# Optimization experiments

Measured on AMD Instinct MI355X. Metric: run time of the kernel, lower is better.

## Reference

```python
import jax, jax.numpy as jnp
import numpy as np
import math

EPS = 1e-20
TEMP = 0.07


def _affinity(x1, x2, n):
    # x1, x2: (B, C, T-1, N+1); use only the first n (non-dustbin) nodes
    A = jnp.einsum('bctn,bctm->btnm', x1[..., :n], x2[..., :n])  # (B,T-1,n,n)
    # entropy of row-normalized affinities (intended math of Categorical(probs=A[b,t,k]).entropy())
    p = A / A.sum(-1, keepdims=True)
    ent = -(p * jnp.log(jnp.maximum(p, EPS))).sum(-1)            # (B,T-1,n)
    dustbin_w = 1.0 / math.log(n)
    A = jnp.concatenate([A, (ent * dustbin_w)[..., None]], axis=-1)  # (B,T-1,n,n+1)
    dust_row = -A.sum(-2)[:, :, None, :]                              # (B,T-1,1,n+1)
    A = jnp.concatenate([A, dust_row], axis=2)                        # (B,T-1,n+1,n+1)
    A = A.at[:, :, -1, -1].set(0.0)
    return A


def _l2norm(x, axis):
    return x / jnp.maximum(jnp.linalg.norm(x, axis=axis, keepdims=True), 1e-12)


def _forward(feats_raw, dust_raw, W_self, b_self, W_dust, b_dust):
    B, N, Cenc, T = feats_raw.shape
    # selfsim head: Linear over channel dim, then L2-normalize features
    f = jnp.einsum('bnct,cd->bndt', feats_raw, W_self) + b_self[None, None, :, None]
    f = _l2norm(f, axis=2)                      # (B,N,128,T)
    q = jnp.transpose(f, (0, 2, 3, 1))          # (B,128,T,N)
    d = jnp.einsum('bct,cd->bdt', dust_raw, W_dust) + b_dust[None, :, None]
    d = _l2norm(d, axis=1)                      # (B,128,T)
    q = jnp.concatenate([q, d[..., None]], axis=-1)  # (B,128,T,N+1)

    Af = _affinity(q[:, :, :-1], q[:, :, 1:], N)
    qf = jnp.flip(q, axis=2)
    Ab = _affinity(qf[:, :, :-1], qf[:, :, 1:], N)

    A12 = jax.nn.softmax(Af / TEMP, axis=-1)    # (B,T-1,M,M)
    A21 = jax.nn.softmax(Ab / TEMP, axis=-1)

    M = N + 1
    tgt = jnp.tile(jnp.arange(M), B)            # (B*M,)
    rows = jnp.arange(B * M)
    left = A12[:, 0]
    right = A21[:, T - 2]
    losses = []
    for i in range(1, T - 1):                   # fixed small loop over time steps
        left = left @ A12[:, i]
        right = A21[:, T - 2 - i] @ right
        AA = left @ right                       # (B,M,M) palindrome walk
        logits = jnp.log(AA + EPS).reshape(-1, M)
        ls = jax.nn.log_softmax(logits, axis=-1)
        losses.append(-ls[rows, tgt].mean())
    loss = sum(losses) / len(losses)
    return q, loss


def setup_inputs() -> dict:
    key = jax.random.key(0)
    ks = jax.random.split(key, 4)
    B, N, C, T, D = 4, 784, 512, 8, 128
    return {
        'feats_raw': jax.random.normal(ks[0], (B, N, C, T), dtype=jnp.float32),
        'dust_raw': jax.random.normal(ks[1], (B, C, T), dtype=jnp.float32),
        'W_self': jax.random.normal(ks[2], (C, D), dtype=jnp.float32) * 0.05,
        'b_self': jnp.zeros((D,), dtype=jnp.float32),
        'W_dust': jax.random.normal(ks[3], (C, D), dtype=jnp.float32) * 0.05,
        'b_dust': jnp.zeros((D,), dtype=jnp.float32),
    }


def reference(feats_raw, dust_raw, W_self, b_self, W_dust, b_dust):
    return _forward(feats_raw, dust_raw, W_self, b_self, W_dust, b_dust)
```

## Files before the change

kernel.cpp:

```cpp
#include <hip/hip_runtime.h>
#include <hip/hip_bf16.h>
#include <math.h>

constexpr int Bc = 4;
constexpr int Nc = 784;
constexpr int Cc = 512;
constexpr int Tc = 8;
constexpr int Dc = 128;
constexpr int Mc = 785;
constexpr int TM1 = 7;
constexpr int Pp = 832;
constexpr int Qrows = 896;
constexpr float TEMP = 0.07f;

typedef __attribute__((ext_vector_type(4))) float f32x4;
typedef __attribute__((ext_vector_type(8))) unsigned short u16x8;
typedef __attribute__((ext_vector_type(8))) __bf16 bf16x8;

__device__ __forceinline__ unsigned short f2bf(float v) {
    __hip_bfloat16 h = __float2bfloat16(v);
    return __builtin_bit_cast(unsigned short, h);
}
__device__ __forceinline__ float bf2f(unsigned short u) {
    return __builtin_bit_cast(float, (unsigned int)u << 16);
}

__device__ __forceinline__ void gload16(const void* g, void* l) {
    __builtin_amdgcn_global_load_lds(
        (const __attribute__((address_space(1))) unsigned int*)g,
        (__attribute__((address_space(3))) unsigned int*)l, 16, 0, 0);
}

template<int LD>
__device__ __forceinline__ void mfma_tile_loop(const unsigned short* __restrict__ A,
                                               const unsigned short* __restrict__ BT,
                                               unsigned short* __restrict__ As,
                                               unsigned short* __restrict__ Bs,
                                               int i0, int j0, int tid,
                                               f32x4 (&acc)[4][4])
{
    const int lane = tid & 63, w = tid >> 6;
    const int wr = w >> 1, wc = w & 1;
    const int g = lane >> 4, lr = lane & 15;

    for (int k0 = 0; k0 < LD; k0 += 64) {
        __syncthreads();
        #pragma unroll
        for (int q = 0; q < 4; ++q) {
            int L16 = q * 256 + tid;
            int r = L16 >> 3;
            int csw = ((L16 & 7) << 4) ^ ((r & 7) << 4);
            const char* ga = (const char*)(A  + (size_t)(i0 + r) * LD + k0) + csw;
            const char* gb = (const char*)(BT + (size_t)(j0 + r) * LD + k0) + csw;
            gload16(ga, As + (size_t)L16 * 8);
            gload16(gb, Bs + (size_t)L16 * 8);
        }
        __syncthreads();
        #pragma unroll
        for (int ks = 0; ks < 2; ++ks) {
            bf16x8 af[4], bf[4];
            #pragma unroll
            for (int m = 0; m < 4; ++m) {
                int r = wr * 64 + m * 16 + lr;
                int cb = (ks * 64 + g * 16) ^ ((r & 7) << 4);
                af[m] = __builtin_bit_cast(bf16x8, *(const u16x8*)((const char*)As + r * 128 + cb));
            }
            #pragma unroll
            for (int n = 0; n < 4; ++n) {
                int r = wc * 64 + n * 16 + lr;
                int cb = (ks * 64 + g * 16) ^ ((r & 7) << 4);
                bf[n] = __builtin_bit_cast(bf16x8, *(const u16x8*)((const char*)Bs + r * 128 + cb));
            }
            #pragma unroll
            for (int m = 0; m < 4; ++m)
                #pragma unroll
                for (int n = 0; n < 4; ++n)
                    acc[m][n] = __builtin_amdgcn_mfma_f32_16x16x32_bf16(af[m], bf[n], acc[m][n], 0, 0, 0);
        }
    }
}

__device__ __forceinline__ float blockReduceSum(float v, float* sbuf) {
    #pragma unroll
    for (int off = 32; off; off >>= 1) v += __shfl_down(v, off, 64);
    __syncthreads();
    if ((threadIdx.x & 63) == 0) sbuf[threadIdx.x >> 6] = v;
    __syncthreads();
    return sbuf[0] + sbuf[1] + sbuf[2] + sbuf[3];
}
__device__ __forceinline__ float blockReduceMax(float v, float* sbuf) {
    #pragma unroll
    for (int off = 32; off; off >>= 1) v = fmaxf(v, __shfl_down(v, off, 64));
    __syncthreads();
    if ((threadIdx.x & 63) == 0) sbuf[threadIdx.x >> 6] = v;
    __syncthreads();
    return fmaxf(fmaxf(sbuf[0], sbuf[1]), fmaxf(sbuf[2], sbuf[3]));
}

__global__ __launch_bounds__(256) void k_pack(const float* __restrict__ feats,
                                              unsigned int* __restrict__ Abf32)
{
    __shared__ float lds[Cc * 9];
    int bid = blockIdx.x;
    int b = bid / Nc, n = bid % Nc;
    const float* src = feats + (size_t)(b * Nc + n) * Cc * Tc;
    int tid = threadIdx.x;
    for (int i = tid; i < Cc * Tc; i += 256) lds[(i >> 3) * 9 + (i & 7)] = src[i];
    __syncthreads();
    #pragma unroll
    for (int t = 0; t < Tc; ++t) {
        size_t row = (size_t)(b * Tc + t) * Nc + n;
        float v0 = lds[(2 * tid) * 9 + t];
        float v1 = lds[(2 * tid + 1) * 9 + t];
        unsigned int pk = (unsigned int)f2bf(v0) | ((unsigned int)f2bf(v1) << 16);
        Abf32[row * (Cc / 2) + tid] = pk;
    }
}

__global__ __launch_bounds__(256) void k_packw(const float* __restrict__ Wself,
                                               const float* __restrict__ Wdust,
                                               unsigned short* __restrict__ WTb)
{
    __shared__ float tile[64][65];
    int which = blockIdx.z;
    const float* W = which ? Wdust : Wself;
    unsigned short* O = WTb + (size_t)which * Dc * Cc;
    int d0 = blockIdx.x * 64, c0 = blockIdx.y * 64;
    int tx = threadIdx.x & 63, ty = threadIdx.x >> 6;
    #pragma unroll
    for (int y = 0; y < 64; y += 4) tile[y + ty][tx] = W[(size_t)(c0 + y + ty) * Dc + d0 + tx];
    __syncthreads();
    #pragma unroll
    for (int y = 0; y < 64; y += 4) O[(size_t)(d0 + y + ty) * Cc + c0 + tx] = f2bf(tile[tx][y + ty]);
}

__global__ __launch_bounds__(256, 3) void k_gemm_proj(const unsigned short* __restrict__ A,
                                                      const unsigned short* __restrict__ BT,
                                                      const float* __restrict__ bias,
                                                      float* __restrict__ Cf)
{
    __shared__ __align__(16) unsigned short As[128 * 64];
    __shared__ __align__(16) unsigned short Bs[128 * 64];
    const int i0 = blockIdx.y * 128;
    const int tid = threadIdx.x, lane = tid & 63, w = tid >> 6;
    const int wr = w >> 1, wc = w & 1;
    const int g = lane >> 4, lr = lane & 15;

    f32x4 acc[4][4] = {};
    mfma_tile_loop<Cc>(A, BT, As, Bs, i0, 0, tid, acc);

    #pragma unroll
    for (int n = 0; n < 4; ++n) {
        int col = wc * 64 + n * 16 + lr;
        float bv = bias[col];
        #pragma unroll
        for (int m = 0; m < 4; ++m)
            #pragma unroll
            for (int j = 0; j < 4; ++j) {
                int row = i0 + wr * 64 + m * 16 + g * 4 + j;
                Cf[(size_t)row * Dc + col] = acc[m][n][j] + bv;
            }
    }
}

__global__ __launch_bounds__(128) void k_dustproj(const float* __restrict__ dust,
                                                  const float* __restrict__ Wdust,
                                                  const float* __restrict__ bdust,
                                                  unsigned short* __restrict__ qTb,
                                                  float* __restrict__ qout)
{
    __shared__ float sdust[Cc];
    __shared__ float red[2];
    int bt = blockIdx.x;
    int b = bt >> 3, t = bt & 7;
    int tid = threadIdx.x;
    for (int i = tid; i < Cc; i += 128) sdust[i] = dust[((size_t)b * Cc + i) * Tc + t];
    __syncthreads();
    float acc = 0.f;
    for (int c = 0; c < Cc; ++c) acc += sdust[c] * Wdust[(size_t)c * Dc + tid];
    acc += bdust[tid];
    float s = acc * acc;
    #pragma unroll
    for (int off = 32; off; off >>= 1) s += __shfl_down(s, off, 64);
    if ((tid & 63) == 0) red[tid >> 6] = s;
    __syncthreads();
    float inv = 1.f / fmaxf(sqrtf(red[0] + red[1]), 1e-12f);
    float qv = acc * inv;
    qTb[((size_t)bt * Qrows + Nc) * Dc + tid] = f2bf(qv);
    qout[(((size_t)b * Dc + tid) * Tc + t) * Mc + Nc] = qv;
}

__global__ __launch_bounds__(256) void k_norm(const float* __restrict__ fbuf,
                                              unsigned short* __restrict__ qTb,
                                              float* __restrict__ qout)
{
    __shared__ float lds[64][129];
    __shared__ float nrm[64][4];
    __shared__ float inv[64];
    int bt = blockIdx.y;
    int b = bt >> 3, t = bt & 7;
    int n0 = blockIdx.x * 64;
    int tid = threadIdx.x;
    #pragma unroll
    for (int q = 0; q < 8; ++q) {
        int i = q * 256 + tid;
        int nl = i >> 5, d4 = i & 31;
        f32x4 v = {};
        if (n0 + nl < Nc) v = *(const f32x4*)(fbuf + ((size_t)bt * Nc + n0 + nl) * Dc + d4 * 4);
        *(f32x4*)(&lds[nl][d4 * 4]) = v;
    }
    __syncthreads();
    {
        int r = tid & 63, p = tid >> 6;
        float s = 0.f;
        #pragma unroll
        for (int j = 0; j < 32; ++j) { float v = lds[r][p * 32 + j]; s += v * v; }
        nrm[r][p] = s;
    }
    __syncthreads();
    if (tid < 64) inv[tid] = 1.f / fmaxf(sqrtf(nrm[tid][0] + nrm[tid][1] + nrm[tid][2] + nrm[tid][3]), 1e-12f);
    __syncthreads();
    unsigned int* qT32 = (unsigned int*)(qTb + (size_t)bt * Qrows * Dc);
    #pragma unroll
    for (int q = 0; q < 16; ++q) {
        int i = q * 256 + tid;
        int nl = i >> 6, dp = i & 63;
        if (n0 + nl < Nc) {
            float iv = inv[nl];
            unsigned int pk = (unsigned int)f2bf(lds[nl][2 * dp] * iv)
                            | ((unsigned int)f2bf(lds[nl][2 * dp + 1] * iv) << 16);
            qT32[((size_t)(n0 + nl) * Dc >> 1) + dp] = pk;
        }
    }
    int nl = tid & 63;
    if (n0 + nl < Nc) {
        float iv = inv[nl];
        #pragma unroll
        for (int dd = 0; dd < Dc; dd += 4) {
            int d = dd + (tid >> 6);
            qout[(((size_t)b * Dc + d) * Tc + t) * Mc + n0 + nl] = lds[nl][d] * iv;
        }
    }
}

__global__ __launch_bounds__(256) void k_affinity(const unsigned short* __restrict__ qTb,
                                                  unsigned short* __restrict__ P12h,
                                                  unsigned short* __restrict__ P21h,
                                                  float* __restrict__ cs12,
                                                  float* __restrict__ cs21,
                                                  float wconst)
{
    constexpr float INVT = 1.0f / TEMP;
    const size_t MMp = (size_t)Pp * Pp;
    int f = blockIdx.x;
    int xcd = f & 7, slot = f >> 3;
    int grp = xcd + 8 * (slot / 49);
    int strip = slot % 49;
    int side = grp >= 28 ? 1 : 0;
    int bt = grp - side * 28;
    int b = bt / TM1, t = bt % TM1;
    const unsigned short *Aq, *Bq;
    unsigned short* OUT;
    float* cs;
    if (side == 0) {
        Aq = qTb + (size_t)(b * Tc + t)     * Qrows * Dc;
        Bq = qTb + (size_t)(b * Tc + t + 1) * Qrows * Dc;
        OUT = P12h + (size_t)bt * MMp;
        cs  = cs12 + (size_t)bt * Pp;
    } else {
        Aq = qTb + (size_t)(b * Tc + 7 - t) * Qrows * Dc;
        Bq = qTb + (size_t)(b * Tc + 6 - t) * Qrows * Dc;
        OUT = P21h + (size_t)bt * MMp;
        cs  = cs21 + (size_t)bt * Pp;
    }
    const int r0 = strip * 16;
    const int tid = threadIdx.x, lane = tid & 63, w = tid >> 6;
    const int g = lane >> 4, lr = lane & 15;

    f32x4 acc[13] = {};
    #pragma unroll
    for (int ks = 0; ks < 4; ++ks) {
        bf16x8 af = __builtin_bit_cast(bf16x8,
            *(const u16x8*)(Aq + (size_t)(r0 + lr) * Dc + ks * 32 + g * 8));
        bf16x8 bfr[7];
        #pragma unroll
        for (int tt = 0; tt < 7; ++tt)
            if (w * 13 + tt < 49)
                bfr[tt] = __builtin_bit_cast(bf16x8,
                    *(const u16x8*)(Bq + (size_t)((w * 13 + tt) * 16 + lr) * Dc + ks * 32 + g * 8));
        #pragma unroll
        for (int tt = 0; tt < 7; ++tt)
            if (w * 13 + tt < 49)
                acc[tt] = __builtin_amdgcn_mfma_f32_16x16x32_bf16(af, bfr[tt], acc[tt], 0, 0, 0);
        #pragma unroll
        for (int tt = 7; tt < 13; ++tt)
            if (w * 13 + tt < 49)
                bfr[tt - 7] = __builtin_bit_cast(bf16x8,
                    *(const u16x8*)(Bq + (size_t)((w * 13 + tt) * 16 + lr) * Dc + ks * 32 + g * 8));
        #pragma unroll
        for (int tt = 7; tt < 13; ++tt)
            if (w * 13 + tt < 49)
                acc[tt] = __builtin_amdgcn_mfma_f32_16x16x32_bf16(af, bfr[tt - 7], acc[tt], 0, 0, 0);
    }

    __shared__ float sred[16][4][2];
    __shared__ float rowsum[16], invZ[16], entP[16];

    float rs[4] = {0.f, 0.f, 0.f, 0.f};
    #pragma unroll
    for (int tt = 0; tt < 13; ++tt) {
        int gt = w * 13 + tt;
        if (gt < 49) {
            float c = 0.f;
            #pragma unroll
            for (int j = 0; j < 4; ++j) {
                float a = acc[tt][j];
                rs[j] += a;
                c += a;
            }
            c += __shfl_xor(c, 16, 64);
            c += __shfl_xor(c, 32, 64);
            if (g == 0) atomicAdd(&cs[gt * 16 + lr], c);
        }
    }
    #pragma unroll
    for (int off = 1; off <= 8; off <<= 1) {
        #pragma unroll
        for (int j = 0; j < 4; ++j) rs[j] += __shfl_xor(rs[j], off, 64);
    }
    if (lr == 0) {
        #pragma unroll
        for (int j = 0; j < 4; ++j) sred[g * 4 + j][w][0] = rs[j];
    }
    __syncthreads();
    if (tid < 16)
        rowsum[tid] = sred[tid][0][0] + sred[tid][1][0] + sred[tid][2][0] + sred[tid][3][0];
    __syncthreads();

    float invr[4];
    #pragma unroll
    for (int j = 0; j < 4; ++j) invr[j] = 1.0f / rowsum[g * 4 + j];
    float en[4] = {0.f, 0.f, 0.f, 0.f}, es[4] = {0.f, 0.f, 0.f, 0.f};
    #pragma unroll
    for (int tt = 0; tt < 13; ++tt) {
        if (w * 13 + tt < 49) {
            #pragma unroll
            for (int j = 0; j < 4; ++j) {
                float a = acc[tt][j];
                float e = __expf(a * INVT);
                es[j] += e;
                float p = a * invr[j];
                en[j] -= p * __logf(fmaxf(p, 1e-20f));
                acc[tt][j] = e;
            }
        }
    }
    #pragma unroll
    for (int off = 1; off <= 8; off <<= 1) {
        #pragma unroll
        for (int j = 0; j < 4; ++j) {
            es[j] += __shfl_xor(es[j], off, 64);
            en[j] += __shfl_xor(en[j], off, 64);
        }
    }
    if (lr == 0) {
        #pragma unroll
        for (int j = 0; j < 4; ++j) { sred[g * 4 + j][w][0] = es[j]; sred[g * 4 + j][w][1] = en[j]; }
    }
    __syncthreads();
    if (tid < 16) {
        float esum = sred[tid][0][0] + sred[tid][1][0] + sred[tid][2][0] + sred[tid][3][0];
        float ent  = sred[tid][0][1] + sred[tid][1][1] + sred[tid][2][1] + sred[tid][3][1];
        float ez  = __expf(ent * wconst * INVT);
        float Z   = esum + ez;
        float iz  = 1.0f / Z;
        invZ[tid] = iz;
        entP[tid] = ez * iz;
    }
    __syncthreads();

    float izl[4];
    #pragma unroll
    for (int j = 0; j < 4; ++j) izl[j] = invZ[g * 4 + j];
    #pragma unroll
    for (int tt = 0; tt < 13; ++tt) {
        int gt = w * 13 + tt;
        int col = gt * 16 + lr;
        #pragma unroll
        for (int j = 0; j < 4; ++j) {
            int row = r0 + g * 4 + j;
            if (gt < 49)
                OUT[(size_t)row * Pp + col] = f2bf(acc[tt][j] * izl[j]);
            else if (col != 784)
                OUT[(size_t)row * Pp + col] = 0;
        }
    }
    if (tid < 16) OUT[(size_t)(r0 + tid) * Pp + 784] = f2bf(entP[tid]);
}

__global__ __launch_bounds__(256) void k_dustrow(const float* __restrict__ cs12,
                                                 const float* __restrict__ cs21,
                                                 unsigned short* __restrict__ P12h,
                                                 unsigned short* __restrict__ P21h)
{
    constexpr float INVT = 1.0f / TEMP;
    const size_t MMp = (size_t)Pp * Pp;
    int bt = blockIdx.x, side = blockIdx.y;
    const float* cs = (side ? cs21 : cs12) + (size_t)bt * Pp;
    unsigned short* OUT = (side ? P21h : P12h) + (size_t)bt * MMp;
    __shared__ float sbuf[4];
    int tid = threadIdx.x;
    float v[4];
    #pragma unroll
    for (int k = 0; k < 4; ++k) {
        int j = tid + k * 256;
        float val = -INFINITY;
        if (j < Nc)       val = -cs[j] * INVT;
        else if (j == Nc) val = 0.f;
        v[k] = val;
    }
    float mx = fmaxf(fmaxf(v[0], v[1]), fmaxf(v[2], v[3]));
    mx = blockReduceMax(mx, sbuf);
    float e[4]; float s = 0.f;
    #pragma unroll
    for (int k = 0; k < 4; ++k) {
        int j = tid + k * 256;
        e[k] = (j < Mc) ? __expf(v[k] - mx) : 0.f;
        s += e[k];
    }
    s = blockReduceSum(s, sbuf);
    float invs = 1.f / s;
    #pragma unroll
    for (int k = 0; k < 4; ++k) {
        int j = tid + k * 256;
        if (j < Mc)      OUT[(size_t)Nc * Pp + j] = f2bf(e[k] * invs);
        else if (j < Pp) OUT[(size_t)Nc * Pp + j] = 0;
    }
    u16x8 z = {};
    u16x8* dst = (u16x8*)(OUT + (size_t)785 * Pp);
    for (int i = tid; i < (Pp - 785) * Pp / 8; i += 256) dst[i] = z;
}

__global__ __launch_bounds__(256) void k_transpose_bf16(const unsigned short* __restrict__ P12h,
                                                        const unsigned short* __restrict__ P21h,
                                                        unsigned short* __restrict__ Db)
{
    const size_t MMp = (size_t)Pp * Pp;
    __shared__ unsigned short tile[64][65];
    int z = blockIdx.z;
    const unsigned short* S;
    if (z < 24) { int b = z / 6, tm = z % 6; S = P12h + ((size_t)b * 7 + tm + 1) * MMp; }
    else        { S = P21h + ((size_t)(z - 24) * 7 + 6) * MMp; }
    unsigned short* D = Db + (size_t)z * MMp;
    int x0 = blockIdx.x * 64, y0 = blockIdx.y * 64;
    int tx = threadIdx.x & 63, ty = threadIdx.x >> 6;
    #pragma unroll
    for (int y = 0; y < 64; y += 4) tile[y + ty][tx] = S[(size_t)(y0 + y + ty) * Pp + x0 + tx];
    __syncthreads();
    #pragma unroll
    for (int y = 0; y < 64; y += 4) D[(size_t)(x0 + y + ty) * Pp + y0 + tx] = tile[tx][y + ty];
}

struct GJobs {
    const unsigned short* A[2];
    const unsigned short* BT[2];
    unsigned short* Cb[2];
    float* cs[2];
    long long sA[2], sB[2], sC[2];
    const unsigned short* Lr;
    const unsigned short* Rr;
    const float* csL;
    float* loss;
    float scale;
};

__global__ __launch_bounds__(256, 3) void k_gemm_loss(GJobs J)
{
    const size_t MMp = (size_t)Pp * Pp;
    if (blockIdx.x >= 392) {
        int q = blockIdx.x - 392;
        int w = threadIdx.x >> 6, lane = threadIdx.x & 63;
        int r = q * 4 + w;
        int b = r / Mc, i = r % Mc;
        const u16x8* lrow = (const u16x8*)(J.Lr + (size_t)b * MMp + (size_t)i * Pp);
        const u16x8* rrow = (const u16x8*)(J.Rr + (size_t)b * MMp + (size_t)i * Pp);
        const f32x4* cs4  = (const f32x4*)(J.csL + (size_t)b * Pp);
        float sR = 0.f, sD = 0.f;
        for (int c = lane; c < Pp / 8; c += 64) {
            u16x8 lv = lrow[c];
            u16x8 rv = rrow[c];
            f32x4 c0 = cs4[2 * c], c1 = cs4[2 * c + 1];
            #pragma unroll
            for (int k = 0; k < 4; ++k) {
                float fl = bf2f(lv[k]);
                sR += fl * c0[k];
                sD += fl * bf2f(rv[k]);
            }
            #pragma unroll
            for (int k = 0; k < 4; ++k) {
                float fl = bf2f(lv[4 + k]);
                sR += fl * c1[k];
                sD += fl * bf2f(rv[4 + k]);
            }
        }
        #pragma unroll
        for (int off = 1; off <= 32; off <<= 1) {
            sR += __shfl_xor(sR, off, 64);
            sD += __shfl_xor(sD, off, 64);
        }
        if (lane == 0)
            atomicAdd(J.loss, (logf(sR + Mc * 1e-20f) - logf(sD + 1e-20f)) * J.scale);
        return;
    }

    __shared__ __align__(16) unsigned short As[128 * 64];
    __shared__ __align__(16) unsigned short Bs[128 * 64];

    int f = blockIdx.x;
    int zz = f & 7, slot = f >> 3;
    int job = zz >> 2, b = zz & 3;
    const unsigned short* A  = J.A[job]  + (size_t)b * J.sA[job];
    const unsigned short* BT = J.BT[job] + (size_t)b * J.sB[job];

    const int i0 = (slot / 7) * 128, j0 = (slot % 7) * 128;
    const int tid = threadIdx.x, lane = tid & 63, w = tid >> 6;
    const int wr = w >> 1, wc = w & 1;
    const int g = lane >> 4, lr = lane & 15;

    f32x4 acc[4][4] = {};
    mfma_tile_loop<Pp>(A, BT, As, Bs, i0, j0, tid, acc);

    unsigned short* Co = J.Cb[job] + (size_t)b * J.sC[job];
    float* csp = J.cs[job];
    float csacc[4] = {0.f, 0.f, 0.f, 0.f};
    #pragma unroll
    for (int m = 0; m < 4; ++m)
        #pragma unroll
        for (int n = 0; n < 4; ++n)
            #pragma unroll
            for (int j = 0; j < 4; ++j) {
                int row = i0 + wr * 64 + m * 16 + g * 4 + j;
                int col = j0 + wc * 64 + n * 16 + lr;
                if (row < Pp && col < Pp) {
                    unsigned short h = f2bf(acc[m][n][j]);
                    Co[(size_t)row * Pp + col] = h;
                    csacc[n] += bf2f(h);
                }
            }
    if (csp) {
        csp += (size_t)b * Pp;
        #pragma unroll
        for (int n = 0; n < 4; ++n) {
            float p = csacc[n];
            p += __shfl_xor(p, 16, 64);
            p += __shfl_xor(p, 32, 64);
            int col = j0 + wc * 64 + n * 16 + lr;
            if (g == 0 && col < Pp) atomicAdd(&csp[col], p);
        }
    }
}

__global__ __launch_bounds__(64) void k_lossrow(const unsigned short* __restrict__ L,
                                                const unsigned short* __restrict__ R,
                                                const float* __restrict__ csR,
                                                float* __restrict__ loss, float scale)
{
    const size_t MMp = (size_t)Pp * Pp;
    int r = blockIdx.x;
    int b = r / Mc, i = r % Mc;
    const u16x8* lrow = (const u16x8*)(L + (size_t)b * MMp + (size_t)i * Pp);
    const u16x8* rrow = (const u16x8*)(R + (size_t)b * MMp + (size_t)i * Pp);
    const f32x4* cs4  = (const f32x4*)(csR + (size_t)b * Pp);
    int lane = threadIdx.x;
    float sR = 0.f, sD = 0.f;
    for (int c = lane; c < Pp / 8; c += 64) {
        u16x8 lv = lrow[c];
        u16x8 rv = rrow[c];
        f32x4 c0 = cs4[2 * c], c1 = cs4[2 * c + 1];
        #pragma unroll
        for (int k = 0; k < 4; ++k) {
            float fl = bf2f(lv[k]);
            sR += fl * c0[k];
            sD += fl * bf2f(rv[k]);
        }
        #pragma unroll
        for (int k = 0; k < 4; ++k) {
            float fl = bf2f(lv[4 + k]);
            sR += fl * c1[k];
            sD += fl * bf2f(rv[4 + k]);
        }
    }
    #pragma unroll
    for (int off = 1; off <= 32; off <<= 1) {
        sR += __shfl_xor(sR, off, 64);
        sD += __shfl_xor(sD, off, 64);
    }
    if (lane == 0)
        atomicAdd(loss, (logf(sR + Mc * 1e-20f) - logf(sD + 1e-20f)) * scale);
}

__global__ void k_zero(float* p) { *p = 0.f; }

extern "C" void kernel_launch(void* const* d_in, const int* in_sizes, int n_in,
                              void* d_out, int out_size, void* d_ws, size_t ws_size,
                              hipStream_t stream)
{
    const float* feats = (const float*)d_in[0];
    const float* dust  = (const float*)d_in[1];
    const float* Wself = (const float*)d_in[2];
    const float* bself = (const float*)d_in[3];
    const float* Wdust = (const float*)d_in[4];
    const float* bdust = (const float*)d_in[5];

    float* out  = (float*)d_out;
    float* qout = out;
    float* loss = out + (size_t)Bc * Dc * Tc * Mc;

    const size_t MMp = (size_t)Pp * Pp;

    float* ws = (float*)d_ws;
    float* csR = ws;
    unsigned short* P12h = (unsigned short*)(ws + 4 * MMp);
    unsigned short* P21h = P12h + (size_t)28 * MMp;
    unsigned short* chainT = P21h + (size_t)28 * MMp;
    unsigned short* P12T  = chainT;
    unsigned short* P21T6 = P12T + (size_t)24 * MMp;
    unsigned short* l0    = P21T6 + (size_t)4 * MMp;
    unsigned short* l1    = l0 + (size_t)4 * MMp;
    unsigned short* R0    = l1 + (size_t)4 * MMp;
    unsigned short* R1    = R0 + (size_t)4 * MMp;
    unsigned short* qTb   = R1 + (size_t)4 * MMp;
    float* cs12 = (float*)(qTb + (size_t)32 * Qrows * Dc);
    float* cs21 = cs12 + (size_t)28 * Pp;

    unsigned short* Abf   = chainT;
    unsigned int*   Abf32 = (unsigned int*)Abf;
    unsigned short* WTb   = Abf + (size_t)Bc * Tc * Nc * Cc;
    float*          fbuf  = (float*)(WTb + 2 * (size_t)Dc * Cc);

    k_pack<<<Bc * Nc, 256, 0, stream>>>(feats, Abf32);
    k_packw<<<dim3(2, 8, 2), 256, 0, stream>>>(Wself, Wdust, WTb);
    hipMemsetAsync(cs12, 0, (size_t)2 * 28 * Pp * sizeof(float), stream);
    hipMemsetAsync(csR, 0, (size_t)6 * Bc * Pp * sizeof(float), stream);
    k_gemm_proj<<<dim3(1, 196), 256, 0, stream>>>(Abf, WTb, bself, fbuf);
    k_dustproj<<<32, 128, 0, stream>>>(dust, Wdust, bdust, qTb, qout);
    k_norm<<<dim3(13, 32), 256, 0, stream>>>(fbuf, qTb, qout);
    float wconst = (float)(1.0 / log(784.0));
    k_affinity<<<2744, 256, 0, stream>>>(qTb, P12h, P21h, cs12, cs21, wconst);
    k_dustrow<<<dim3(28, 2), 256, 0, stream>>>(cs12, cs21, P12h, P21h);
    k_transpose_bf16<<<dim3(13, 13, 28), 256, 0, stream>>>(P12h, P21h, P12T);

    k_zero<<<1, 1, 0, stream>>>(loss);
    const float scale = 1.0f / (6.0f * Bc * Mc);

    {
        GJobs J = {};
        J.A[0] = P12h;  J.sA[0] = (long long)7 * MMp;
        J.BT[0] = P12T; J.sB[0] = (long long)6 * MMp;
        J.Cb[0] = l0;   J.sC[0] = (long long)MMp; J.cs[0] = nullptr;
        J.A[1] = P21T6;                   J.sA[1] = (long long)MMp;
        J.BT[1] = P21h + (size_t)5 * MMp; J.sB[1] = (long long)7 * MMp;
        J.Cb[1] = R0;   J.sC[1] = (long long)MMp; J.cs[1] = csR;
        k_gemm_loss<<<392, 256, 0, stream>>>(J);
    }

    unsigned short *lcur = l0, *lnxt = l1, *rcur = R0, *rnxt = R1;
    for (int i = 1; i <= 5; ++i) {
        GJobs J = {};
        J.A[0] = lcur; J.sA[0] = (long long)MMp;
        J.BT[0] = P12T + (size_t)i * MMp; J.sB[0] = (long long)6 * MMp;
        J.Cb[0] = lnxt; J.sC[0] = (long long)MMp; J.cs[0] = nullptr;
        J.A[1] = rcur; J.sA[1] = (long long)MMp;
        J.BT[1] = P21h + (size_t)(5 - i) * MMp; J.sB[1] = (long long)7 * MMp;
        J.Cb[1] = rnxt; J.sC[1] = (long long)MMp; J.cs[1] = csR + (size_t)i * Bc * Pp;
        J.Lr = lcur; J.Rr = rcur; J.csL = csR + (size_t)(i - 1) * Bc * Pp;
        J.loss = loss; J.scale = scale;
        k_gemm_loss<<<392 + 785, 256, 0, stream>>>(J);
        unsigned short* t;
        t = lcur; lcur = lnxt; lnxt = t;
        t = rcur; rcur = rnxt; rnxt = t;
    }
    k_lossrow<<<Bc * Mc, 64, 0, stream>>>(lcur, rcur, csR + (size_t)5 * Bc * Pp, loss, scale);
}
```

Measured before the change: 507.5 us.

## Stage affinity output tile in LDS and derive column sums from flipped row sums

k_affinity now writes its bf16 output strip into a shared-memory tile and stores it to global memory with 16-byte vector stores, replacing scattered 2-byte stores. The per-column atomicAdd sums are dropped. The forward affinity matrix is the transpose of the backward one at the mirrored time step, so its column sums equal that matrix's row sums, which are written directly into the opposite cs buffer. This removes the cs memset, and the k_zero launch is replaced by a memset. The cost is about 27KB of extra LDS per block, which may reduce occupancy.

```diff
diff --git a/kernel.cpp b/kernel.cpp
--- a/kernel.cpp
+++ b/kernel.cpp
@@ -252,6 +252,10 @@
 {
     constexpr float INVT = 1.0f / TEMP;
     const size_t MMp = (size_t)Pp * Pp;
+    __shared__ unsigned short otile[16][840];
+    __shared__ float sred[16][4][2];
+    __shared__ float rowsum[16], invZ[16], entP[16];
+
     int f = blockIdx.x;
     int xcd = f & 7, slot = f >> 3;
     int grp = xcd + 8 * (slot / 49);
@@ -261,18 +265,17 @@
     int b = bt / TM1, t = bt % TM1;
     const unsigned short *Aq, *Bq;
     unsigned short* OUT;
-    float* cs;
     if (side == 0) {
         Aq = qTb + (size_t)(b * Tc + t)     * Qrows * Dc;
         Bq = qTb + (size_t)(b * Tc + t + 1) * Qrows * Dc;
         OUT = P12h + (size_t)bt * MMp;
-        cs  = cs12 + (size_t)bt * Pp;
     } else {
         Aq = qTb + (size_t)(b * Tc + 7 - t) * Qrows * Dc;
         Bq = qTb + (size_t)(b * Tc + 6 - t) * Qrows * Dc;
         OUT = P21h + (size_t)bt * MMp;
-        cs  = cs21 + (size_t)bt * Pp;
-    }
+    }
+    float* csFlip = (side == 0 ? cs21 : cs12) + (size_t)(b * TM1 + (6 - t)) * Pp;
+
     const int r0 = strip * 16;
     const int tid = threadIdx.x, lane = tid & 63, w = tid >> 6;
     const int g = lane >> 4, lr = lane & 15;
@@ -303,24 +306,12 @@
                 acc[tt] = __builtin_amdgcn_mfma_f32_16x16x32_bf16(af, bfr[tt - 7], acc[tt], 0, 0, 0);
     }
 
-    __shared__ float sred[16][4][2];
-    __shared__ float rowsum[16], invZ[16], entP[16];
-
     float rs[4] = {0.f, 0.f, 0.f, 0.f};
     #pragma unroll
     for (int tt = 0; tt < 13; ++tt) {
-        int gt = w * 13 + tt;
-        if (gt < 49) {
-            float c = 0.f;
-            #pragma unroll
-            for (int j = 0; j < 4; ++j) {
-                float a = acc[tt][j];
-                rs[j] += a;
-                c += a;
-            }
-            c += __shfl_xor(c, 16, 64);
-            c += __shfl_xor(c, 32, 64);
-            if (g == 0) atomicAdd(&cs[gt * 16 + lr], c);
+        if (w * 13 + tt < 49) {
+            #pragma unroll
+            for (int j = 0; j < 4; ++j) rs[j] += acc[tt][j];
         }
     }
     #pragma unroll
@@ -333,8 +324,11 @@
         for (int j = 0; j < 4; ++j) sred[g * 4 + j][w][0] = rs[j];
     }
     __syncthreads();
-    if (tid < 16)
-        rowsum[tid] = sred[tid][0][0] + sred[tid][1][0] + sred[tid][2][0] + sred[tid][3][0];
+    if (tid < 16) {
+        float r = sred[tid][0][0] + sred[tid][1][0] + sred[tid][2][0] + sred[tid][3][0];
+        rowsum[tid] = r;
+        csFlip[r0 + tid] = r;
+    }
     __syncthreads();
 
     float invr[4];
@@ -385,17 +379,21 @@
     #pragma unroll
     for (int tt = 0; tt < 13; ++tt) {
         int gt = w * 13 + tt;
-        int col = gt * 16 + lr;
-        #pragma unroll
-        for (int j = 0; j < 4; ++j) {
-            int row = r0 + g * 4 + j;
-            if (gt < 49)
-                OUT[(size_t)row * Pp + col] = f2bf(acc[tt][j] * izl[j]);
-            else if (col != 784)
-                OUT[(size_t)row * Pp + col] = 0;
-        }
-    }
-    if (tid < 16) OUT[(size_t)(r0 + tid) * Pp + 784] = f2bf(entP[tid]);
+        if (gt < 49) {
+            int col = gt * 16 + lr;
+            #pragma unroll
+            for (int j = 0; j < 4; ++j)
+                otile[g * 4 + j][col] = f2bf(acc[tt][j] * izl[j]);
+        }
+    }
+    if (tid < 16) otile[tid][784] = f2bf(entP[tid]);
+    for (int i = tid; i < 16 * 47; i += 256) otile[i / 47][785 + i % 47] = 0;
+    __syncthreads();
+
+    for (int v = tid; v < 16 * 104; v += 256) {
+        int row = v / 104, cv = v % 104;
+        *(u16x8*)(OUT + (size_t)(r0 + row) * Pp + cv * 8) = *(const u16x8*)(&otile[row][cv * 8]);
+    }
 }
 
 __global__ __launch_bounds__(256) void k_dustrow(const float* __restrict__ cs12,
@@ -599,8 +597,6 @@
         atomicAdd(loss, (logf(sR + Mc * 1e-20f) - logf(sD + 1e-20f)) * scale);
 }
 
-__global__ void k_zero(float* p) { *p = 0.f; }
-
 extern "C" void kernel_launch(void* const* d_in, const int* in_sizes, int n_in,
                               void* d_out, int out_size, void* d_ws, size_t ws_size,
                               hipStream_t stream)
@@ -640,8 +636,8 @@
 
     k_pack<<<Bc * Nc, 256, 0, stream>>>(feats, Abf32);
     k_packw<<<dim3(2, 8, 2), 256, 0, stream>>>(Wself, Wdust, WTb);
-    hipMemsetAsync(cs12, 0, (size_t)2 * 28 * Pp * sizeof(float), stream);
     hipMemsetAsync(csR, 0, (size_t)6 * Bc * Pp * sizeof(float), stream);
+    hipMemsetAsync(loss, 0, sizeof(float), stream);
     k_gemm_proj<<<dim3(1, 196), 256, 0, stream>>>(Abf, WTb, bself, fbuf);
     k_dustproj<<<32, 128, 0, stream>>>(dust, Wdust, bdust, qTb, qout);
     k_norm<<<dim3(13, 32), 256, 0, stream>>>(fbuf, qTb, qout);
@@ -650,7 +646,6 @@
     k_dustrow<<<dim3(28, 2), 256, 0, stream>>>(cs12, cs21, P12h, P21h);
     k_transpose_bf16<<<dim3(13, 13, 28), 256, 0, stream>>>(P12h, P21h, P12T);
 
-    k_zero<<<1, 1, 0, stream>>>(loss);
     const float scale = 1.0f / (6.0f * Bc * Mc);
 
     {
```

Result: faster. 497.5 us (-2.0%).
